# Kernel tuning notes

Measured on AMD Instinct MI355X. Metric: run time of the kernel, lower is better.

The kernel has to match this reference:

```python
import jax, jax.numpy as jnp
import numpy as np

N = 50000; E = 800000; B = 500; L = 42
F_IN = 35; HEADS = 10; F_H = 35; F_G = 350
VOCAB = 26; EMB = 128; NF = 16; OUT_DIM = 128; K = 8
NEG_SLOPE = 0.2


def setup_inputs() -> dict:
    key = jax.random.key(0)
    ks = jax.random.split(key, 16)
    inp = {}
    inp['x'] = jax.random.normal(ks[0], (N, F_IN), jnp.float32)
    inp['edge_index'] = jax.random.randint(ks[1], (2, E), 0, N, dtype=jnp.int32)
    inp['batch'] = jnp.sort(jax.random.randint(ks[2], (N,), 0, B, dtype=jnp.int32))
    inp['target'] = jax.random.randint(ks[3], (B, L), 0, VOCAB, dtype=jnp.int32)
    # --- learned parameters ---
    inp['W_gat'] = jax.random.normal(ks[4], (F_IN, HEADS * F_H), jnp.float32) * 0.1
    inp['att_src'] = jax.random.normal(ks[5], (HEADS, F_H), jnp.float32) * 0.1
    inp['att_dst'] = jax.random.normal(ks[6], (HEADS, F_H), jnp.float32) * 0.1
    inp['b_gat'] = jnp.zeros((HEADS * F_H,), jnp.float32)
    inp['W_gcn'] = jax.random.normal(ks[7], (F_G, F_G), jnp.float32) * 0.05
    inp['b_gcn'] = jnp.zeros((F_G,), jnp.float32)
    inp['W_fcg1'] = jax.random.normal(ks[8], (2 * F_G, 1500), jnp.float32) * 0.03
    inp['b_fcg1'] = jnp.zeros((1500,), jnp.float32)
    inp['W_fcg2'] = jax.random.normal(ks[9], (1500, OUT_DIM), jnp.float32) * 0.03
    inp['b_fcg2'] = jnp.zeros((OUT_DIM,), jnp.float32)
    inp['emb_xt'] = jax.random.normal(ks[10], (VOCAB, EMB), jnp.float32) * 0.1
    inp['W_conv'] = jax.random.normal(ks[11], (NF, EMB, K), jnp.float32) * 0.05
    inp['b_conv'] = jnp.zeros((NF,), jnp.float32)
    inp['W_fcxt'] = jax.random.normal(ks[12], (NF * 35, OUT_DIM), jnp.float32) * 0.05
    inp['b_fcxt'] = jnp.zeros((OUT_DIM,), jnp.float32)
    inp['W_fc1'] = jax.random.normal(ks[13], (256, 512), jnp.float32) * 0.05
    inp['b_fc1'] = jnp.zeros((512,), jnp.float32)
    inp['W_out'] = jax.random.normal(ks[14], (512, 1), jnp.float32) * 0.05
    inp['b_out'] = jnp.zeros((1,), jnp.float32)
    return inp


def _add_self_loops(edge_index):
    loop = jnp.arange(N, dtype=edge_index.dtype)
    src = jnp.concatenate([edge_index[0], loop])
    dst = jnp.concatenate([edge_index[1], loop])
    return src, dst


def _gat_conv(x, src, dst, W, att_src, att_dst, b):
    # h: [N, H, C]
    h = (x @ W).reshape(N, HEADS, F_H)
    a_s = jnp.einsum('nhc,hc->nh', h, att_src)  # [N, H]
    a_d = jnp.einsum('nhc,hc->nh', h, att_dst)
    e = jax.nn.leaky_relu(a_s[src] + a_d[dst], NEG_SLOPE)  # [Etot, H]
    # segment softmax over incoming edges per destination node, per head
    m = jax.ops.segment_max(e, dst, num_segments=N)
    m = jnp.where(jnp.isfinite(m), m, 0.0)
    ex = jnp.exp(e - m[dst])
    den = jax.ops.segment_sum(ex, dst, num_segments=N)
    alpha = ex / (den[dst] + 1e-16)  # [Etot, H]
    out = jax.ops.segment_sum(h[src] * alpha[:, :, None], dst, num_segments=N)
    return out.reshape(N, HEADS * F_H) + b, alpha


def _gcn_conv(x, src, dst, W, b):
    deg = jax.ops.segment_sum(jnp.ones_like(dst, jnp.float32), dst, num_segments=N)
    dinv = jnp.where(deg > 0, deg ** -0.5, 0.0)
    norm = dinv[src] * dinv[dst]  # symmetric normalization
    h = x @ W
    return jax.ops.segment_sum(h[src] * norm[:, None], dst, num_segments=N) + b


def reference(x, edge_index, batch, target, W_gat, att_src, att_dst, b_gat,
              W_gcn, b_gcn, W_fcg1, b_fcg1, W_fcg2, b_fcg2, emb_xt,
              W_conv, b_conv, W_fcxt, b_fcxt, W_fc1, b_fc1, W_out, b_out):
    src, dst = _add_self_loops(edge_index)
    # --- graph branch ---
    xg, alpha = _gat_conv(x, src, dst, W_gat, att_src, att_dst, b_gat)
    xg = jax.nn.relu(xg)
    xg = jax.nn.relu(_gcn_conv(xg, src, dst, W_gcn, b_gcn))
    # global max + mean pool per graph
    gmax = jax.ops.segment_max(xg, batch, num_segments=B)
    gsum = jax.ops.segment_sum(xg, batch, num_segments=B)
    cnt = jax.ops.segment_sum(jnp.ones((N,), jnp.float32), batch, num_segments=B)
    gmean = gsum / jnp.maximum(cnt, 1.0)[:, None]
    xg = jnp.concatenate([gmax, gmean], axis=1)  # [B, 700]
    xg = jax.nn.relu(xg @ W_fcg1 + b_fcg1)
    xg = xg @ W_fcg2 + b_fcg2  # [B, 128] (dropout is identity in eval)
    # --- protein branch ---
    emb = emb_xt[target]                      # [B, L, 128]
    emb = jnp.transpose(emb, (0, 2, 1))       # [B, 128, L]
    conv = jax.lax.conv_general_dilated(
        emb, W_conv, window_strides=(1,), padding='VALID',
        dimension_numbers=('NCH', 'OIH', 'NCH'))  # [B, 16, 35]
    conv = conv + b_conv[None, :, None]
    xt = conv.reshape(B, NF * 35)
    xt = xt @ W_fcxt + b_fcxt                 # [B, 128]
    # --- fusion ---
    xc = jnp.concatenate([xg, xt], axis=1)    # [B, 256]
    xc = jax.nn.relu(xc @ W_fc1 + b_fc1)
    out = jax.nn.sigmoid(xc @ W_out + b_out)  # [B, 1]
    return out, alpha
```

## Files before the change

### kernel.cpp

```cpp
#include <hip/hip_runtime.h>
#include <math.h>

#define NN 50000
#define EE 800000
#define BB 500
#define LL 42
#define NHEAD 10
#define FH 35
#define FG 350
#define ETOT (EE + NN)
#define NCHUNK ((NN + 511) / 512)

#define KPAD 384
#define LDH2 352
#define MPAD 50048
#define MB2  512
#define NDW  24

typedef unsigned short ushort_t;
typedef __attribute__((ext_vector_type(8))) short short8v;
typedef __attribute__((ext_vector_type(4))) float float4v;

__device__ __forceinline__ float lrelu(float x) { return x > 0.f ? x : 0.2f * x; }

__device__ __forceinline__ ushort_t f2bf(float f) {
    unsigned int u = __float_as_uint(f);
    u += 0x7fffu + ((u >> 16) & 1u);
    return (ushort_t)(u >> 16);
}
__device__ __forceinline__ float bflo(unsigned u) { return __uint_as_float(u << 16); }
__device__ __forceinline__ float bfhi(unsigned u) { return __uint_as_float(u & 0xffff0000u); }
__device__ __forceinline__ float bfu(ushort_t u) { return __uint_as_float(((unsigned)u) << 16); }
__device__ __forceinline__ unsigned packbf(float a, float b) {
    return (unsigned)f2bf(a) | ((unsigned)f2bf(b) << 16);
}

__device__ __forceinline__ void async_cp16(const void* g, void* l) {
    __builtin_amdgcn_global_load_lds((const __attribute__((address_space(1))) unsigned int*)g,
                                     (__attribute__((address_space(3))) unsigned int*)l, 16, 0, 0);
}

__global__ __launch_bounds__(256) void k_init(int* deg, int* cur) {
    int i = blockIdx.x * 256 + threadIdx.x;
    if (i < NN) { deg[i] = 1; cur[i] = 0; }
}

__global__ __launch_bounds__(256) void k_deg(const int* __restrict__ ei, int* deg) {
    int i = blockIdx.x * 256 + threadIdx.x;
    if (i < EE) atomicAdd(&deg[ei[EE + i]], 1);
}

__global__ __launch_bounds__(512) void k_scan1(const int* __restrict__ deg, int* part) {
    int i = blockIdx.x * 512 + threadIdx.x;
    int lane = threadIdx.x & 63, wv = threadIdx.x >> 6;
    int x = (i < NN) ? deg[i] : 0;
    #pragma unroll
    for (int d = 32; d; d >>= 1) x += __shfl_xor(x, d);
    __shared__ int wsum[8];
    if (lane == 0) wsum[wv] = x;
    __syncthreads();
    if (threadIdx.x == 0) {
        int s = 0;
        #pragma unroll
        for (int w = 0; w < 8; w++) s += wsum[w];
        part[blockIdx.x] = s;
    }
}

__global__ __launch_bounds__(64) void k_scan2(const int* __restrict__ part, int* pscan) {
    int l = threadIdx.x;
    int v0 = (l < NCHUNK) ? part[l] : 0;
    #pragma unroll
    for (int d = 1; d < 64; d <<= 1) { int t = __shfl_up(v0, d); if (l >= d) v0 += t; }
    int tot0 = __shfl(v0, 63);
    int v1 = (64 + l < NCHUNK) ? part[64 + l] : 0;
    #pragma unroll
    for (int d = 1; d < 64; d <<= 1) { int t = __shfl_up(v1, d); if (l >= d) v1 += t; }
    v1 += tot0;
    if (l < NCHUNK) pscan[l] = v0;
    if (64 + l < NCHUNK) pscan[64 + l] = v1;
}

__global__ __launch_bounds__(512) void k_scan3(const int* __restrict__ deg, const int* __restrict__ pscan,
                                               int* offs, float* dinv) {
    int i = blockIdx.x * 512 + threadIdx.x;
    int lane = threadIdx.x & 63, wv = threadIdx.x >> 6;
    int x = (i < NN) ? deg[i] : 0;
    int incl = x;
    #pragma unroll
    for (int d = 1; d < 64; d <<= 1) { int t = __shfl_up(incl, d); if (lane >= d) incl += t; }
    __shared__ int wtot[8];
    if (lane == 63) wtot[wv] = incl;
    __syncthreads();
    int woff = 0;
    for (int w = 0; w < wv; w++) woff += wtot[w];
    int base = (blockIdx.x == 0) ? 0 : pscan[blockIdx.x - 1];
    if (i < NN) {
        offs[i] = base + woff + incl - x;
        dinv[i] = rsqrtf((float)x);
    }
}

__global__ __launch_bounds__(256) void k_scatter(const int* __restrict__ ei, const int* __restrict__ offs,
                                                 int* cur, int* csr_src) {
    int i = blockIdx.x * 256 + threadIdx.x;
    if (i < EE) {
        int s = ei[i], d = ei[EE + i];
        int slot = atomicAdd(&cur[d], 1);
        csr_src[offs[d] + slot] = s;
    } else if (i < ETOT) {
        int v = i - EE;
        int slot = atomicAdd(&cur[v], 1);
        csr_src[offs[v] + slot] = v;
    }
}

__global__ __launch_bounds__(256) void k_prep_att(const float* __restrict__ W_gat, const float* __restrict__ att_s,
                                                  const float* __restrict__ att_d,
                                                  float* __restrict__ wS, float* __restrict__ wD) {
    int i = blockIdx.x * 256 + threadIdx.x;
    if (i >= FG) return;
    int hd = i / 35, c = i % 35;
    float ss = 0.f, dd = 0.f;
    for (int cc = 0; cc < 35; cc++) {
        float w = W_gat[c * FG + hd * 35 + cc];
        ss += w * att_s[hd * 35 + cc];
        dd += w * att_d[hd * 35 + cc];
    }
    wS[i] = ss;
    wD[i] = dd;
}

__global__ __launch_bounds__(256) void k_prep_node(const float* __restrict__ x, const float* __restrict__ wS,
                                                   const float* __restrict__ wD, ushort_t* __restrict__ nd,
                                                   float* __restrict__ a_s, float* __restrict__ a_d) {
    __shared__ float sw[FG], dw[FG];
    int tid = threadIdx.x;
    for (int i = tid; i < FG; i += 256) { sw[i] = wS[i]; dw[i] = wD[i]; }
    __syncthreads();
    int n = blockIdx.x * 256 + tid;
    if (n >= NN) return;
    float xr[35];
    #pragma unroll
    for (int c = 0; c < 35; c++) xr[c] = x[(size_t)n * 35 + c];
    unsigned* xo = (unsigned*)(nd + (size_t)n * (2 * NDW));
    #pragma unroll
    for (int w = 0; w < 17; w++) xo[w] = packbf(xr[2 * w], xr[2 * w + 1]);
    xo[17] = packbf(xr[34], 0.f);
    float asv[NHEAD];
    #pragma unroll
    for (int hd = 0; hd < NHEAD; hd++) {
        const float* ws = &sw[hd * 35];
        const float* wd = &dw[hd * 35];
        float as = 0.f, ad = 0.f;
        #pragma unroll
        for (int c = 0; c < 35; c++) { float v = xr[c]; as += v * ws[c]; ad += v * wd[c]; }
        asv[hd] = as;
        a_s[n * NHEAD + hd] = as;
        a_d[n * NHEAD + hd] = ad;
    }
    #pragma unroll
    for (int j = 0; j < 5; j++) xo[18 + j] = packbf(asv[2 * j], asv[2 * j + 1]);
    xo[23] = 0u;
}

__global__ __launch_bounds__(256) void k_prep_weights(
    const float* __restrict__ Wg, const float* __restrict__ Wc,
    const float* __restrict__ W1, const float* __restrict__ W2,
    const float* __restrict__ WX, const float* __restrict__ WF,
    ushort_t* __restrict__ BD, ushort_t* __restrict__ GC,
    ushort_t* __restrict__ F1, ushort_t* __restrict__ F2,
    ushort_t* __restrict__ FX, ushort_t* __restrict__ FC) {
    int i = blockIdx.x * 256 + threadIdx.x;
    if (i < KPAD * KPAD) {
        int n = i / KPAD, k = i % KPAD;
        int hd = k / 36, cc = k % 36;
        float v = 0.f;
        if (n < FG && cc < 35 && hd == n / 35) v = Wg[cc * FG + n];
        BD[i] = f2bf(v);
        return;
    }
    i -= KPAD * KPAD;
    if (i < KPAD * KPAD) {
        int n = i / KPAD, k = i % KPAD;
        float v = (n < FG && k < FG) ? Wc[k * FG + n] : 0.f;
        GC[i] = f2bf(v);
        return;
    }
    i -= KPAD * KPAD;
    if (i < 704 * 1536) {
        int k = i / 1536, n = i % 1536;
        float v = (k < 700 && n < 1500) ? W1[(size_t)k * 1500 + n] : 0.f;
        F1[(size_t)n * 704 + k] = f2bf(v);
        return;
    }
    i -= 704 * 1536;
    if (i < 1536 * 128) {
        int k = i / 128, n = i % 128;
        float v = (k < 1500) ? W2[(size_t)k * 128 + n] : 0.f;
        F2[(size_t)n * 1536 + k] = f2bf(v);
        return;
    }
    i -= 1536 * 128;
    if (i < 576 * 128) {
        int k = i / 128, n = i % 128;
        float v = (k < 560) ? WX[(size_t)k * 128 + n] : 0.f;
        FX[(size_t)n * 576 + k] = f2bf(v);
        return;
    }
    i -= 576 * 128;
    if (i < 256 * 512) {
        int k = i / 512, n = i % 512;
        FC[(size_t)n * 256 + k] = f2bf(WF[(size_t)k * 512 + n]);
    }
}
#define PREPW_TOTAL (KPAD * KPAD * 2 + 704 * 1536 + 1536 * 128 + 576 * 128 + 256 * 512)

__global__ __launch_bounds__(256) void k_cast_pad(const float* __restrict__ src, ushort_t* __restrict__ dst,
                                                  int M, int K, int MP, int KP) {
    int i = blockIdx.x * 256 + threadIdx.x;
    if (i >= MP * KP) return;
    int r = i / KP, k = i % KP;
    dst[i] = (r < M && k < K) ? f2bf(src[(size_t)r * K + k]) : (ushort_t)0;
}

__global__ __launch_bounds__(256) void k_mfma(const ushort_t* __restrict__ A, const ushort_t* __restrict__ Bt,
                                              void* __restrict__ C, int M, int Nv, int ldc, int lda,
                                              int ksteps, const float* __restrict__ bias, int act, int bf16out,
                                              int bdiag, int nst) {
    __shared__ ushort_t As[128 * 64];
    __shared__ ushort_t Bs[64 * 64];
    int tid = threadIdx.x;
    int wid = tid >> 6, lane = tid & 63;
    int m0 = blockIdx.y * 128, n0 = blockIdx.x * 64;
    int wm0 = (wid >> 1) * 64, wn0 = (wid & 1) * 32;
    int srow = tid >> 3;
    int scol = (tid & 7) * 8;
    float4v acc[4][2] = {{{0.f,0.f,0.f,0.f},{0.f,0.f,0.f,0.f}},
                         {{0.f,0.f,0.f,0.f},{0.f,0.f,0.f,0.f}},
                         {{0.f,0.f,0.f,0.f},{0.f,0.f,0.f,0.f}},
                         {{0.f,0.f,0.f,0.f},{0.f,0.f,0.f,0.f}}};
    int a_off = (wm0 + (lane & 15)) * 64 + (lane >> 4) * 8;
    int b_off = (wn0 + (lane & 15)) * 64 + (lane >> 4) * 8;
    int ks0 = 0, ks1 = ksteps;
    if (bdiag) {
        int hlo = n0 / 35;
        int hhi = (n0 + 63) / 35; if (hhi > 9) hhi = 9;
        ks0 = (hlo * 36) >> 6;
        ks1 = (hhi * 36 + 36 + 63) >> 6;
    }
    for (int ks = ks0; ks < ks1; ks++) {
        int k0 = ks * 64;
        #pragma unroll
        for (int r = 0; r < 4; r++) {
            const ushort_t* g = A + (size_t)(m0 + r * 32 + srow) * lda + k0 + scol;
            async_cp16(g, As + (r * 256 + tid) * 8);
        }
        #pragma unroll
        for (int r = 0; r < 2; r++) {
            const ushort_t* g = Bt + (size_t)(n0 + r * 32 + srow) * lda + k0 + scol;
            async_cp16(g, Bs + (r * 256 + tid) * 8);
        }
        __syncthreads();
        #pragma unroll
        for (int kh = 0; kh < 2; kh++) {
            short8v b0 = *(const short8v*)&Bs[b_off + kh * 32];
            short8v b1 = *(const short8v*)&Bs[b_off + 16 * 64 + kh * 32];
            #pragma unroll
            for (int mi = 0; mi < 4; mi++) {
                short8v a = *(const short8v*)&As[a_off + mi * 16 * 64 + kh * 32];
                acc[mi][0] = __builtin_amdgcn_mfma_f32_16x16x32_bf16(a, b0, acc[mi][0], 0, 0, 0);
                acc[mi][1] = __builtin_amdgcn_mfma_f32_16x16x32_bf16(a, b1, acc[mi][1], 0, 0, 0);
            }
        }
        __syncthreads();
    }
    int lm = m0 + wm0 + (lane >> 4) * 4;
    int lc = n0 + wn0 + (lane & 15);
    #pragma unroll
    for (int mi = 0; mi < 4; mi++) {
        #pragma unroll
        for (int ni = 0; ni < 2; ni++) {
            int col = lc + ni * 16;
            if (col >= nst) continue;
            float bv = (bias != nullptr && col < Nv) ? bias[col] : 0.f;
            #pragma unroll
            for (int r = 0; r < 4; r++) {
                int row = lm + mi * 16 + r;
                if (row >= M) continue;
                float v = acc[mi][ni][r] + bv;
                if (act) v = fmaxf(v, 0.f);
                if (col >= Nv) v = 0.f;
                if (bf16out) ((ushort_t*)C)[(size_t)row * ldc + col] = f2bf(v);
                else         ((float*)C)[(size_t)row * ldc + col] = v;
            }
        }
    }
}

__global__ __launch_bounds__(128) void k_gat_agg(const ushort_t* __restrict__ nd,
                                                 const float* __restrict__ a_d,
                                                 const int* __restrict__ csr_src,
                                                 const int* __restrict__ offs, const int* __restrict__ deg,
                                                 ushort_t* __restrict__ Zb, float* __restrict__ denArr) {
    int wid = blockIdx.x * 2 + (threadIdx.x >> 6);
    int lane = threadIdx.x & 63;
    if (wid >= MPAD) return;
    unsigned* zr = (unsigned*)(Zb + (size_t)wid * KPAD);
    if (wid >= NN) {
        __builtin_nontemporal_store(0u, &zr[lane]);
        __builtin_nontemporal_store(0u, &zr[lane + 64]);
        __builtin_nontemporal_store(0u, &zr[lane + 128]);
        return;
    }
    int o0 = offs[wid], d = deg[wid];
    int h1 = lane / 18,        c1 = lane % 18;
    int h2 = (lane + 64) / 18, c2 = (lane + 64) % 18;
    bool g3 = lane < 52;
    int h3 = g3 ? (lane + 128) / 18 : 7;
    int c3 = g3 ? (lane + 128) % 18 : 0;
    float adv1 = a_d[wid * NHEAD + h1];
    float adv2 = a_d[wid * NHEAD + h2];
    float adv3 = a_d[wid * NHEAD + h3];
    float den1 = 0.f, den2 = 0.f, den3 = 0.f;
    float a1l = 0.f, a1h = 0.f, a2l = 0.f, a2h = 0.f, a3l = 0.f, a3h = 0.f;
    int i = 0;
    for (; i + 4 <= d; i += 4) {
        int s[4];
        #pragma unroll
        for (int j = 0; j < 4; j++) s[j] = csr_src[o0 + i + j];
        ushort_t w1[4], w2[4], w3[4];
        unsigned u1[4], u2[4], u3[4];
        #pragma unroll
        for (int j = 0; j < 4; j++) {
            const ushort_t* r = nd + (size_t)s[j] * (2 * NDW);
            w1[j] = r[36 + h1]; w2[j] = r[36 + h2]; w3[j] = r[36 + h3];
            const unsigned* ru = (const unsigned*)r;
            u1[j] = ru[c1]; u2[j] = ru[c2]; u3[j] = ru[c3];
        }
        #pragma unroll
        for (int j = 0; j < 4; j++) {
            float e1 = __expf(lrelu(bfu(w1[j]) + adv1));
            float e2 = __expf(lrelu(bfu(w2[j]) + adv2));
            float e3 = __expf(lrelu(bfu(w3[j]) + adv3));
            den1 += e1; den2 += e2; den3 += e3;
            a1l += e1 * bflo(u1[j]); a1h += e1 * bfhi(u1[j]);
            a2l += e2 * bflo(u2[j]); a2h += e2 * bfhi(u2[j]);
            a3l += e3 * bflo(u3[j]); a3h += e3 * bfhi(u3[j]);
        }
    }
    for (; i < d; i++) {
        int s = csr_src[o0 + i];
        const ushort_t* r = nd + (size_t)s * (2 * NDW);
        const unsigned* ru = (const unsigned*)r;
        float e1 = __expf(lrelu(bfu(r[36 + h1]) + adv1));
        float e2 = __expf(lrelu(bfu(r[36 + h2]) + adv2));
        float e3 = __expf(lrelu(bfu(r[36 + h3]) + adv3));
        den1 += e1; den2 += e2; den3 += e3;
        a1l += e1 * bflo(ru[c1]); a1h += e1 * bfhi(ru[c1]);
        a2l += e2 * bflo(ru[c2]); a2h += e2 * bfhi(ru[c2]);
        a3l += e3 * bflo(ru[c3]); a3h += e3 * bfhi(ru[c3]);
    }
    float* dw = denArr + (size_t)wid * NHEAD;
    if (lane == 0)  { dw[0] = den1; dw[7] = den3; }
    if (lane == 18) dw[1] = den1;
    if (lane == 36) dw[2] = den1;
    if (lane == 54) dw[3] = den1;
    if (lane == 8)  dw[4] = den2;
    if (lane == 26) dw[5] = den2;
    if (lane == 44) dw[6] = den2;
    if (lane == 16) dw[8] = den3;
    if (lane == 34) dw[9] = den3;
    float r1 = 1.f / (den1 + 1e-16f);
    float r2 = 1.f / (den2 + 1e-16f);
    float r3 = 1.f / (den3 + 1e-16f);
    __builtin_nontemporal_store(packbf(a1l * r1, a1h * r1), &zr[lane]);
    __builtin_nontemporal_store(packbf(a2l * r2, a2h * r2), &zr[lane + 64]);
    __builtin_nontemporal_store(g3 ? packbf(a3l * r3, a3h * r3) : 0u, &zr[lane + 128]);
}

__global__ __launch_bounds__(256) void k_alpha(const int* __restrict__ ei, const float* __restrict__ a_s,
                                               const float* __restrict__ a_d, const float* __restrict__ den,
                                               float* __restrict__ alphaOut) {
    int i = blockIdx.x * 256 + threadIdx.x;
    if (i >= ETOT * NHEAD) return;
    int e = i / NHEAD, hd = i % NHEAD;
    int s, dst;
    if (e < EE) { s = ei[e]; dst = ei[EE + e]; }
    else { s = dst = e - EE; }
    float zs = bfu(f2bf(a_s[s * NHEAD + hd]));
    float ex = __expf(lrelu(zs + a_d[dst * NHEAD + hd]));
    __builtin_nontemporal_store(ex / (den[dst * NHEAD + hd] + 1e-16f), &alphaOut[i]);
}

__global__ __launch_bounds__(128) void k_gcn_agg(const ushort_t* __restrict__ h2b,
                                                 const int* __restrict__ csr_src,
                                                 const int* __restrict__ offs, const int* __restrict__ deg,
                                                 const float* __restrict__ dinv, const float* __restrict__ b_gcn,
                                                 ushort_t* __restrict__ xg2b) {
    int wid = blockIdx.x * 2 + (threadIdx.x >> 6);
    int lane = threadIdx.x & 63;
    if (wid >= NN) return;
    int o0 = offs[wid], d = deg[wid];
    float wv = dinv[wid];
    bool g3 = lane < 48;
    int w3 = g3 ? (lane + 128) : 0;
    float aL0 = 0.f, aH0 = 0.f, aL1 = 0.f, aH1 = 0.f, aL2 = 0.f, aH2 = 0.f;
    const unsigned* h32 = (const unsigned*)h2b;
    int i = 0;
    for (; i + 8 <= d; i += 8) {
        int s[8];
        #pragma unroll
        for (int j = 0; j < 8; j++) s[j] = csr_src[o0 + i + j];
        float q[8]; unsigned ua[8], ub[8], uc[8];
        #pragma unroll
        for (int j = 0; j < 8; j++) {
            q[j] = dinv[s[j]];
            const unsigned* hr = h32 + (size_t)s[j] * (LDH2 / 2);
            ua[j] = hr[lane]; ub[j] = hr[lane + 64]; uc[j] = hr[w3];
        }
        #pragma unroll
        for (int j = 0; j < 8; j++) {
            aL0 += q[j] * bflo(ua[j]); aH0 += q[j] * bfhi(ua[j]);
            aL1 += q[j] * bflo(ub[j]); aH1 += q[j] * bfhi(ub[j]);
            aL2 += q[j] * bflo(uc[j]); aH2 += q[j] * bfhi(uc[j]);
        }
    }
    for (; i < d; i++) {
        int s = csr_src[o0 + i];
        float ws = dinv[s];
        const unsigned* hr = h32 + (size_t)s * (LDH2 / 2);
        unsigned u0 = hr[lane], u1 = hr[lane + 64], u2 = hr[w3];
        aL0 += ws * bflo(u0);  aH0 += ws * bfhi(u0);
        aL1 += ws * bflo(u1);  aH1 += ws * bfhi(u1);
        aL2 += ws * bflo(u2);  aH2 += ws * bfhi(u2);
    }
    unsigned* orow = (unsigned*)(xg2b + (size_t)wid * FG);
    {
        int f = 2 * lane;
        __builtin_nontemporal_store(packbf(fmaxf(wv * aL0 + b_gcn[f], 0.f),
                                           fmaxf(wv * aH0 + b_gcn[f + 1], 0.f)), &orow[lane]);
    }
    {
        int f = 128 + 2 * lane;
        __builtin_nontemporal_store(packbf(fmaxf(wv * aL1 + b_gcn[f], 0.f),
                                           fmaxf(wv * aH1 + b_gcn[f + 1], 0.f)), &orow[64 + lane]);
    }
    if (lane < 47) {
        int f = 256 + 2 * lane;
        __builtin_nontemporal_store(packbf(fmaxf(wv * aL2 + b_gcn[f], 0.f),
                                           fmaxf(wv * aH2 + b_gcn[f + 1], 0.f)), &orow[128 + lane]);
    }
}

__device__ __forceinline__ int lowerB(const int* a, int n, int key) {
    int lo = 0, hi = n;
    while (lo < hi) { int mid = (lo + hi) >> 1; if (a[mid] < key) lo = mid + 1; else hi = mid; }
    return lo;
}

__global__ __launch_bounds__(256) void k_pool(const ushort_t* __restrict__ xg2b, const int* __restrict__ batch,
                                              float* __restrict__ pooled) {
    int g = blockIdx.x;
    int w = threadIdx.x;
    if (w >= 175) return;
    int s = lowerB(batch, NN, g);
    int e = lowerB(batch, NN, g + 1);
    const unsigned* base = (const unsigned*)xg2b;
    float mx0 = -INFINITY, mx1 = -INFINITY, sm0 = 0.f, sm1 = 0.f;
    int n = s;
    for (; n + 2 <= e; n += 2) {
        unsigned ua = base[(size_t)n * 175 + w];
        unsigned ub = base[(size_t)(n + 1) * 175 + w];
        float a0 = bflo(ua), a1 = bfhi(ua), b0 = bflo(ub), b1 = bfhi(ub);
        mx0 = fmaxf(mx0, fmaxf(a0, b0));
        mx1 = fmaxf(mx1, fmaxf(a1, b1));
        sm0 += a0 + b0;
        sm1 += a1 + b1;
    }
    for (; n < e; n++) {
        unsigned ua = base[(size_t)n * 175 + w];
        float a0 = bflo(ua), a1 = bfhi(ua);
        mx0 = fmaxf(mx0, a0);
        mx1 = fmaxf(mx1, a1);
        sm0 += a0;
        sm1 += a1;
    }
    float rc = 1.f / fmaxf((float)(e - s), 1.f);
    pooled[g * 700 + 2 * w]       = mx0;
    pooled[g * 700 + 2 * w + 1]   = mx1;
    pooled[g * 700 + FG + 2 * w]     = sm0 * rc;
    pooled[g * 700 + FG + 2 * w + 1] = sm1 * rc;
}

__global__ __launch_bounds__(256) void k_conv(const int* __restrict__ target, const float* __restrict__ emb,
                                              const float* __restrict__ Wc, const float* __restrict__ bc,
                                              float* __restrict__ xt) {
    __shared__ float embL[26 * 132];
    __shared__ float WL[16 * 8 * 128];
    __shared__ int   tgL[2 * LL];
    int tid = threadIdx.x;
    int b0 = blockIdx.x * 2;
    for (int i = tid; i < 26 * 128; i += 256) {
        int r = i >> 7, e = i & 127;
        embL[r * 132 + e] = emb[i];
    }
    for (int i = tid; i < 16384; i += 256) {
        int f = i >> 10, rem = i & 1023, k = rem >> 7, e = rem & 127;
        WL[i] = Wc[f * 1024 + e * 8 + k];
    }
    if (tid < 2 * LL) tgL[tid] = target[b0 * LL + tid];
    __syncthreads();
    #pragma unroll
    for (int pass = 0; pass < 2; pass++) {
        int r = tid + pass * 256;
        if (r >= 280) break;
        int bl = r / 140, rem = r % 140;
        int fq = rem / 35, t = rem % 35;
        const int* tg = &tgL[bl * LL];
        float ac0 = 0.f, ac1 = 0.f, ac2 = 0.f, ac3 = 0.f;
        for (int k = 0; k < 8; k++) {
            const float* er = &embL[tg[t + k] * 132];
            const float* w0 = &WL[((fq * 4 + 0) * 8 + k) * 128];
            const float* w1 = &WL[((fq * 4 + 1) * 8 + k) * 128];
            const float* w2 = &WL[((fq * 4 + 2) * 8 + k) * 128];
            const float* w3 = &WL[((fq * 4 + 3) * 8 + k) * 128];
            #pragma unroll 8
            for (int e = 0; e < 128; e += 4) {
                float4 a = *(const float4*)&er[e];
                float4 q0 = *(const float4*)&w0[e];
                float4 q1 = *(const float4*)&w1[e];
                float4 q2 = *(const float4*)&w2[e];
                float4 q3 = *(const float4*)&w3[e];
                ac0 += a.x * q0.x + a.y * q0.y + a.z * q0.z + a.w * q0.w;
                ac1 += a.x * q1.x + a.y * q1.y + a.z * q1.z + a.w * q1.w;
                ac2 += a.x * q2.x + a.y * q2.y + a.z * q2.z + a.w * q2.w;
                ac3 += a.x * q3.x + a.y * q3.y + a.z * q3.z + a.w * q3.w;
            }
        }
        int b = b0 + bl, fb = fq * 4;
        xt[b * 560 + (fb + 0) * 35 + t] = ac0 + bc[fb + 0];
        xt[b * 560 + (fb + 1) * 35 + t] = ac1 + bc[fb + 1];
        xt[b * 560 + (fb + 2) * 35 + t] = ac2 + bc[fb + 2];
        xt[b * 560 + (fb + 3) * 35 + t] = ac3 + bc[fb + 3];
    }
}

__global__ __launch_bounds__(256) void k_out(const float* __restrict__ f1, const float* __restrict__ W_out,
                                             const float* __restrict__ b_out, float* __restrict__ out) {
    int wid = (blockIdx.x * blockDim.x + threadIdx.x) >> 6;
    int lane = threadIdx.x & 63;
    if (wid >= BB) return;
    const float* xr = f1 + (size_t)wid * 512;
    float acc = 0.f;
    #pragma unroll
    for (int k = 0; k < 8; k++) acc += xr[lane + k * 64] * W_out[lane + k * 64];
    #pragma unroll
    for (int d = 32; d; d >>= 1) acc += __shfl_xor(acc, d);
    if (lane == 0) out[wid] = 1.f / (1.f + __expf(-(acc + b_out[0])));
}

extern "C" void kernel_launch(void* const* d_in, const int* in_sizes, int n_in,
                              void* d_out, int out_size, void* d_ws, size_t ws_size,
                              hipStream_t stream) {
    const float* x      = (const float*)d_in[0];
    const int*   ei     = (const int*)d_in[1];
    const int*   batch  = (const int*)d_in[2];
    const int*   target = (const int*)d_in[3];
    const float* W_gat  = (const float*)d_in[4];
    const float* att_s  = (const float*)d_in[5];
    const float* att_d  = (const float*)d_in[6];
    const float* b_gat  = (const float*)d_in[7];
    const float* W_gcn  = (const float*)d_in[8];
    const float* b_gcn  = (const float*)d_in[9];
    const float* W_fcg1 = (const float*)d_in[10];
    const float* b_fcg1 = (const float*)d_in[11];
    const float* W_fcg2 = (const float*)d_in[12];
    const float* b_fcg2 = (const float*)d_in[13];
    const float* embxt  = (const float*)d_in[14];
    const float* W_conv = (const float*)d_in[15];
    const float* b_conv = (const float*)d_in[16];
    const float* W_fcxt = (const float*)d_in[17];
    const float* b_fcxt = (const float*)d_in[18];
    const float* W_fc1  = (const float*)d_in[19];
    const float* b_fc1  = (const float*)d_in[20];
    const float* W_out  = (const float*)d_in[21];
    const float* b_out  = (const float*)d_in[22];

    float* out_sig  = (float*)d_out;
    float* alphaOut = (float*)d_out + BB;

    size_t o = 0;
    auto alloc = [&](size_t bytes) -> void* {
        o = (o + 255) & ~(size_t)255;
        void* p = (char*)d_ws + o;
        o += bytes;
        return p;
    };
    int*   deg     = (int*)alloc((size_t)NN * 4);
    int*   cur     = (int*)alloc((size_t)NN * 4);
    int*   offs    = (int*)alloc((size_t)NN * 4);
    int*   part    = (int*)alloc(128 * 4);
    int*   pscan   = (int*)alloc(128 * 4);
    int*   csr_src = (int*)alloc((size_t)ETOT * 4);
    float* dinv    = (float*)alloc((size_t)NN * 4);
    float* a_s     = (float*)alloc((size_t)NN * NHEAD * 4);
    float* a_d     = (float*)alloc((size_t)NN * NHEAD * 4);
    float* denArr  = (float*)alloc((size_t)NN * NHEAD * 4);
    ushort_t* nd   = (ushort_t*)alloc((size_t)NN * 48 * 2);
    float* wS      = (float*)alloc((size_t)FG * 4);
    float* wD      = (float*)alloc((size_t)FG * 4);
    ushort_t* WtBD = (ushort_t*)alloc((size_t)KPAD * KPAD * 2);
    ushort_t* WtGC = (ushort_t*)alloc((size_t)KPAD * KPAD * 2);
    ushort_t* WtF1 = (ushort_t*)alloc((size_t)1536 * 704 * 2);
    ushort_t* WtF2 = (ushort_t*)alloc((size_t)128 * 1536 * 2);
    ushort_t* WtFX = (ushort_t*)alloc((size_t)128 * 576 * 2);
    ushort_t* WtFC = (ushort_t*)alloc((size_t)512 * 256 * 2);
    float* pooled  = (float*)alloc((size_t)BB * 700 * 4);
    ushort_t* pooledb = (ushort_t*)alloc((size_t)MB2 * 704 * 2);
    ushort_t* t1b  = (ushort_t*)alloc((size_t)MB2 * 1536 * 2);
    float* xt      = (float*)alloc((size_t)BB * 560 * 4);
    ushort_t* xtb  = (ushort_t*)alloc((size_t)MB2 * 576 * 2);
    ushort_t* xcb  = (ushort_t*)alloc((size_t)MB2 * 256 * 2);
    float* f1      = (float*)alloc((size_t)MB2 * 512 * 4);
    ushort_t* hb   = (ushort_t*)alloc((size_t)MPAD * KPAD * 2);
    char*  R2      = (char*)alloc((size_t)NN * FG * 4);
    ushort_t* xg1b = (ushort_t*)R2;
    ushort_t* xg2b = (ushort_t*)R2;
    (void)ws_size; (void)n_in; (void)in_sizes; (void)out_size;

    auto mfma = [&](const ushort_t* A, const ushort_t* Bt, void* C, const float* bias,
                    int M2, int Nv, int NP, int ldc, int KP, int act, int bf16out, int bdiag, int nst) {
        dim3 g(NP / 64, M2 / 128);
        k_mfma<<<g, 256, 0, stream>>>(A, Bt, C, M2, Nv, ldc, KP, KP / 64, bias, act, bf16out, bdiag, nst);
    };

    k_init<<<(NN + 255) / 256, 256, 0, stream>>>(deg, cur);
    k_deg<<<(EE + 255) / 256, 256, 0, stream>>>(ei, deg);
    k_scan1<<<NCHUNK, 512, 0, stream>>>(deg, part);
    k_scan2<<<1, 64, 0, stream>>>(part, pscan);
    k_scan3<<<NCHUNK, 512, 0, stream>>>(deg, pscan, offs, dinv);
    k_scatter<<<(ETOT + 255) / 256, 256, 0, stream>>>(ei, offs, cur, csr_src);

    k_prep_att<<<2, 256, 0, stream>>>(W_gat, att_s, att_d, wS, wD);
    k_prep_node<<<(NN + 255) / 256, 256, 0, stream>>>(x, wS, wD, nd, a_s, a_d);
    k_prep_weights<<<(PREPW_TOTAL + 255) / 256, 256, 0, stream>>>(W_gat, W_gcn, W_fcg1, W_fcg2,
                                                                  W_fcxt, W_fc1,
                                                                  WtBD, WtGC, WtF1, WtF2, WtFX, WtFC);

    k_gat_agg<<<MPAD / 2, 128, 0, stream>>>(nd, a_d, csr_src, offs, deg, hb, denArr);
    k_alpha<<<(ETOT * NHEAD + 255) / 256, 256, 0, stream>>>(ei, a_s, a_d, denArr, alphaOut);
    mfma(hb, WtBD, xg1b, b_gat, MPAD, FG, KPAD, KPAD, KPAD, 1, 1, 1, KPAD);

    mfma(xg1b, WtGC, hb, nullptr, MPAD, FG, KPAD, LDH2, KPAD, 0, 1, 0, LDH2);
    k_gcn_agg<<<(NN + 1) / 2, 128, 0, stream>>>(hb, csr_src, offs, deg, dinv, b_gcn, xg2b);

    k_pool<<<BB, 256, 0, stream>>>(xg2b, batch, pooled);
    k_cast_pad<<<(MB2 * 704 + 255) / 256, 256, 0, stream>>>(pooled, pooledb, BB, 700, MB2, 704);
    mfma(pooledb, WtF1, t1b, b_fcg1, MB2, 1500, 1536, 1536, 704, 1, 1, 0, 1536);
    mfma(t1b, WtF2, xcb, b_fcg2, MB2, 128, 128, 256, 1536, 0, 1, 0, 128);
    k_conv<<<250, 256, 0, stream>>>(target, embxt, W_conv, b_conv, xt);
    k_cast_pad<<<(MB2 * 576 + 255) / 256, 256, 0, stream>>>(xt, xtb, BB, 560, MB2, 576);
    mfma(xtb, WtFX, xcb + 128, b_fcxt, MB2, 128, 128, 256, 576, 0, 1, 0, 128);
    mfma(xcb, WtFC, f1, b_fc1, MB2, 512, 512, 512, 256, 1, 0, 0, 512);
    k_out<<<(BB + 3) / 4, 256, 0, stream>>>(f1, W_out, b_out, out_sig);
}
```

Before: 575.5 us.

## Factor GAT attention exponentials per node and pad rows to power-of-two strides

Precomputes exp(a_s) and exp(0.2*a_s) per source node and exp(a_d) terms per destination. This turns each per-edge exp(leaky_relu(a_s+a_d)) into two multiplies and a select, in both the aggregation and alpha kernels. It also widens the node record to 64 bf16 and the GCN intermediate row stride to 512 elements, so row addressing becomes shifts and rows align to cache lines. The trade-offs are larger gather footprints and memory, plus a risk of overflow or precision loss when exponentials are stored in bf16 before multiplying.

Result: no change. 580.0 us (+0.8%).

```diff
diff --git a/kernel.cpp b/kernel.cpp
--- a/kernel.cpp
+++ b/kernel.cpp
@@ -12,10 +12,10 @@
 #define NCHUNK ((NN + 511) / 512)
 
 #define KPAD 384
-#define LDH2 352
+#define LDH2 512
 #define MPAD 50048
 #define MB2  512
-#define NDW  24
+#define NDW  32
 
 typedef unsigned short ushort_t;
 typedef __attribute__((ext_vector_type(8))) short short8v;
@@ -143,11 +143,10 @@
     float xr[35];
     #pragma unroll
     for (int c = 0; c < 35; c++) xr[c] = x[(size_t)n * 35 + c];
-    unsigned* xo = (unsigned*)(nd + (size_t)n * (2 * NDW));
+    unsigned* xo = (unsigned*)(nd + ((size_t)n << 6));
     #pragma unroll
     for (int w = 0; w < 17; w++) xo[w] = packbf(xr[2 * w], xr[2 * w + 1]);
     xo[17] = packbf(xr[34], 0.f);
-    float asv[NHEAD];
     #pragma unroll
     for (int hd = 0; hd < NHEAD; hd++) {
         const float* ws = &sw[hd * 35];
@@ -155,13 +154,11 @@
         float as = 0.f, ad = 0.f;
         #pragma unroll
         for (int c = 0; c < 35; c++) { float v = xr[c]; as += v * ws[c]; ad += v * wd[c]; }
-        asv[hd] = as;
         a_s[n * NHEAD + hd] = as;
         a_d[n * NHEAD + hd] = ad;
-    }
-    #pragma unroll
-    for (int j = 0; j < 5; j++) xo[18 + j] = packbf(asv[2 * j], asv[2 * j + 1]);
-    xo[23] = 0u;
+        xo[18 + hd] = packbf(__expf(as), __expf(0.2f * as));
+    }
+    xo[28] = 0u; xo[29] = 0u; xo[30] = 0u; xo[31] = 0u;
 }
 
 __global__ __launch_bounds__(256) void k_prep_weights(
@@ -319,30 +316,35 @@
     bool g3 = lane < 52;
     int h3 = g3 ? (lane + 128) / 18 : 7;
     int c3 = g3 ? (lane + 128) % 18 : 0;
-    float adv1 = a_d[wid * NHEAD + h1];
-    float adv2 = a_d[wid * NHEAD + h2];
-    float adv3 = a_d[wid * NHEAD + h3];
+    float ad1 = a_d[wid * NHEAD + h1];
+    float ad2 = a_d[wid * NHEAD + h2];
+    float ad3 = a_d[wid * NHEAD + h3];
+    float ev1 = __expf(ad1), ev1b = __expf(0.2f * ad1);
+    float ev2 = __expf(ad2), ev2b = __expf(0.2f * ad2);
+    float ev3 = __expf(ad3), ev3b = __expf(0.2f * ad3);
     float den1 = 0.f, den2 = 0.f, den3 = 0.f;
     float a1l = 0.f, a1h = 0.f, a2l = 0.f, a2h = 0.f, a3l = 0.f, a3h = 0.f;
+    const unsigned* x32 = (const unsigned*)nd;
     int i = 0;
     for (; i + 4 <= d; i += 4) {
         int s[4];
         #pragma unroll
         for (int j = 0; j < 4; j++) s[j] = csr_src[o0 + i + j];
-        ushort_t w1[4], w2[4], w3[4];
-        unsigned u1[4], u2[4], u3[4];
+        unsigned p1[4], p2[4], p3[4], u1[4], u2[4], u3[4];
         #pragma unroll
         for (int j = 0; j < 4; j++) {
-            const ushort_t* r = nd + (size_t)s[j] * (2 * NDW);
-            w1[j] = r[36 + h1]; w2[j] = r[36 + h2]; w3[j] = r[36 + h3];
-            const unsigned* ru = (const unsigned*)r;
-            u1[j] = ru[c1]; u2[j] = ru[c2]; u3[j] = ru[c3];
+            const unsigned* r = x32 + ((size_t)s[j] << 5);
+            p1[j] = r[18 + h1]; p2[j] = r[18 + h2]; p3[j] = r[18 + h3];
+            u1[j] = r[c1]; u2[j] = r[c2]; u3[j] = r[c3];
         }
         #pragma unroll
         for (int j = 0; j < 4; j++) {
-            float e1 = __expf(lrelu(bfu(w1[j]) + adv1));
-            float e2 = __expf(lrelu(bfu(w2[j]) + adv2));
-            float e3 = __expf(lrelu(bfu(w3[j]) + adv3));
+            float e1p = bflo(p1[j]) * ev1, e1n = bfhi(p1[j]) * ev1b;
+            float e2p = bflo(p2[j]) * ev2, e2n = bfhi(p2[j]) * ev2b;
+            float e3p = bflo(p3[j]) * ev3, e3n = bfhi(p3[j]) * ev3b;
+            float e1 = (e1p > 1.f) ? e1p : e1n;
+            float e2 = (e2p > 1.f) ? e2p : e2n;
+            float e3 = (e3p > 1.f) ? e3p : e3n;
             den1 += e1; den2 += e2; den3 += e3;
             a1l += e1 * bflo(u1[j]); a1h += e1 * bfhi(u1[j]);
             a2l += e2 * bflo(u2[j]); a2h += e2 * bfhi(u2[j]);
@@ -351,15 +353,19 @@
     }
     for (; i < d; i++) {
         int s = csr_src[o0 + i];
-        const ushort_t* r = nd + (size_t)s * (2 * NDW);
-        const unsigned* ru = (const unsigned*)r;
-        float e1 = __expf(lrelu(bfu(r[36 + h1]) + adv1));
-        float e2 = __expf(lrelu(bfu(r[36 + h2]) + adv2));
-        float e3 = __expf(lrelu(bfu(r[36 + h3]) + adv3));
+        const unsigned* r = x32 + ((size_t)s << 5);
+        unsigned p1v = r[18 + h1], p2v = r[18 + h2], p3v = r[18 + h3];
+        unsigned u1v = r[c1], u2v = r[c2], u3v = r[c3];
+        float e1p = bflo(p1v) * ev1, e1n = bfhi(p1v) * ev1b;
+        float e2p = bflo(p2v) * ev2, e2n = bfhi(p2v) * ev2b;
+        float e3p = bflo(p3v) * ev3, e3n = bfhi(p3v) * ev3b;
+        float e1 = (e1p > 1.f) ? e1p : e1n;
+        float e2 = (e2p > 1.f) ? e2p : e2n;
+        float e3 = (e3p > 1.f) ? e3p : e3n;
         den1 += e1; den2 += e2; den3 += e3;
-        a1l += e1 * bflo(ru[c1]); a1h += e1 * bfhi(ru[c1]);
-        a2l += e2 * bflo(ru[c2]); a2h += e2 * bfhi(ru[c2]);
-        a3l += e3 * bflo(ru[c3]); a3h += e3 * bfhi(ru[c3]);
+        a1l += e1 * bflo(u1v); a1h += e1 * bfhi(u1v);
+        a2l += e2 * bflo(u2v); a2h += e2 * bfhi(u2v);
+        a3l += e3 * bflo(u3v); a3h += e3 * bfhi(u3v);
     }
     float* dw = denArr + (size_t)wid * NHEAD;
     if (lane == 0)  { dw[0] = den1; dw[7] = den3; }
@@ -388,8 +394,13 @@
     int s, dst;
     if (e < EE) { s = ei[e]; dst = ei[EE + e]; }
     else { s = dst = e - EE; }
-    float zs = bfu(f2bf(a_s[s * NHEAD + hd]));
-    float ex = __expf(lrelu(zs + a_d[dst * NHEAD + hd]));
+    float as = a_s[s * NHEAD + hd];
+    float ad = a_d[dst * NHEAD + hd];
+    float eas  = bfu(f2bf(__expf(as)));
+    float eas2 = bfu(f2bf(__expf(0.2f * as)));
+    float ep = eas * __expf(ad);
+    float en = eas2 * __expf(0.2f * ad);
+    float ex = (ep > 1.f) ? ep : en;
     __builtin_nontemporal_store(ex / (den[dst * NHEAD + hd] + 1e-16f), &alphaOut[i]);
 }
 
@@ -416,7 +427,7 @@
         #pragma unroll
         for (int j = 0; j < 8; j++) {
             q[j] = dinv[s[j]];
-            const unsigned* hr = h32 + (size_t)s[j] * (LDH2 / 2);
+            const unsigned* hr = h32 + ((size_t)s[j] << 8);
             ua[j] = hr[lane]; ub[j] = hr[lane + 64]; uc[j] = hr[w3];
         }
         #pragma unroll
@@ -429,7 +440,7 @@
     for (; i < d; i++) {
         int s = csr_src[o0 + i];
         float ws = dinv[s];
-        const unsigned* hr = h32 + (size_t)s * (LDH2 / 2);
+        const unsigned* hr = h32 + ((size_t)s << 8);
         unsigned u0 = hr[lane], u1 = hr[lane + 64], u2 = hr[w3];
         aL0 += ws * bflo(u0);  aH0 += ws * bfhi(u0);
         aL1 += ws * bflo(u1);  aH1 += ws * bfhi(u1);
@@ -607,7 +618,7 @@
     float* a_s     = (float*)alloc((size_t)NN * NHEAD * 4);
     float* a_d     = (float*)alloc((size_t)NN * NHEAD * 4);
     float* denArr  = (float*)alloc((size_t)NN * NHEAD * 4);
-    ushort_t* nd   = (ushort_t*)alloc((size_t)NN * 48 * 2);
+    ushort_t* nd   = (ushort_t*)alloc((size_t)NN * 64 * 2);
     float* wS      = (float*)alloc((size_t)FG * 4);
     float* wD      = (float*)alloc((size_t)FG * 4);
     ushort_t* WtBD = (ushort_t*)alloc((size_t)KPAD * KPAD * 2);
@@ -623,7 +634,7 @@
     ushort_t* xtb  = (ushort_t*)alloc((size_t)MB2 * 576 * 2);
     ushort_t* xcb  = (ushort_t*)alloc((size_t)MB2 * 256 * 2);
     float* f1      = (float*)alloc((size_t)MB2 * 512 * 4);
-    ushort_t* hb   = (ushort_t*)alloc((size_t)MPAD * KPAD * 2);
+    ushort_t* hb   = (ushort_t*)alloc((size_t)MPAD * LDH2 * 2);
     char*  R2      = (char*)alloc((size_t)NN * FG * 4);
     ushort_t* xg1b = (ushort_t*)R2;
     ushort_t* xg2b = (ushort_t*)R2;
@@ -652,7 +663,7 @@
     k_alpha<<<(ETOT * NHEAD + 255) / 256, 256, 0, stream>>>(ei, a_s, a_d, denArr, alphaOut);
     mfma(hb, WtBD, xg1b, b_gat, MPAD, FG, KPAD, KPAD, KPAD, 1, 1, 1, KPAD);
 
-    mfma(xg1b, WtGC, hb, nullptr, MPAD, FG, KPAD, LDH2, KPAD, 0, 1, 0, LDH2);
+    mfma(xg1b, WtGC, hb, nullptr, MPAD, FG, KPAD, LDH2, KPAD, 0, 1, 0, 352);
     k_gcn_agg<<<(NN + 1) / 2, 128, 0, stream>>>(hb, csr_src, offs, deg, dinv, b_gcn, xg2b);
 
     k_pool<<<BB, 256, 0, stream>>>(xg2b, batch, pooled);
```
